# Kernel optimization log

Hardware: AMD Instinct MI355X
Metric: run time of the kernel (lower is better)

## Reference

```python
import jax, jax.numpy as jnp
import numpy as np

B, CH, N = 4, 128, 4096
PC = CH // 2  # pos channels = 64


def setup_inputs() -> dict:
    key = jax.random.key(0)
    ks = jax.random.split(key, 6)
    s_p = 1.0 / np.sqrt(PC)
    s_v = 1.0 / np.sqrt(CH)
    return {
        "pos_bot": jax.random.normal(ks[0], (B, PC, N), dtype=jnp.float32),
        "corr_feats": jax.random.normal(ks[1], (B, CH, N), dtype=jnp.float32),
        "Wp": jax.random.uniform(ks[2], (PC, PC), jnp.float32, -s_p, s_p),
        "bp": jax.random.uniform(ks[3], (PC,), jnp.float32, -s_p, s_p),
        "Wv": jax.random.uniform(ks[4], (CH, CH), jnp.float32, -s_v, s_v),
        "bv": jax.random.uniform(ks[5], (CH,), jnp.float32, -s_v, s_v),
        "beta": jnp.asarray([1.0], dtype=jnp.float32),
    }


def reference(pos_bot, corr_feats, Wp, bp, Wv, bv, beta):
    # 1x1 Conv1d == per-position matmul over channels
    pos = jnp.einsum("oc,bcn->bon", Wp, pos_bot) + bp[None, :, None]      # [B,64,N]
    value = jnp.einsum("oc,bcn->bon", Wv, corr_feats) + bv[None, :, None]  # [B,128,N]

    x = jnp.transpose(pos, (0, 2, 1))  # [B,N,64]
    # squared euclidean pairwise distance: ||xi||^2 + ||xj||^2 - 2 xi.xj
    sq = jnp.sum(x * x, axis=-1)  # [B,N]
    d2 = sq[:, :, None] + sq[:, None, :] - 2.0 * jnp.einsum("bnd,bmd->bnm", x, x)
    d2 = jnp.maximum(d2, 0.0)
    kernel = jnp.exp(-d2 * beta[0])  # [B,N,N] Gaussian RBF

    equation_F = jnp.transpose(value, (0, 2, 1))  # [B,N,128]
    return kernel, equation_F
```

## Files before the change

### kernel.cpp

```cpp
#include <hip/hip_runtime.h>
#include <hip/hip_bf16.h>

typedef _Float16 f16x8 __attribute__((ext_vector_type(8)));
typedef _Float16 f16x4 __attribute__((ext_vector_type(4)));
typedef float    f32x4 __attribute__((ext_vector_type(4)));

constexpr int BB = 4;
constexpr int CH = 128;
constexpr int PC = 64;
constexpr int NN = 4096;

__global__ __launch_bounds__(256) void proj_kernel(
    const float* __restrict__ pos_bot,
    const float* __restrict__ corr,
    const float* __restrict__ Wp,
    const float* __restrict__ bp,
    const float* __restrict__ Wv,
    const float* __restrict__ bv,
    _Float16* __restrict__ xbuf,
    float*    __restrict__ sq,
    float*    __restrict__ eqF)
{
    const int tid  = threadIdx.x;
    const int wid  = tid >> 6;
    const int lane = tid & 63;
    const int l15  = lane & 15;
    const int lg   = lane >> 4;
    const int b    = blockIdx.y & 3;
    const int n    = blockIdx.x * 16 + l15;

    if ((blockIdx.y >> 2) == 0) {
        const int mt = wid;
        f16x8 wf[2], pb[2];
#pragma unroll
        for (int ks = 0; ks < 2; ++ks) {
            const float* wp = Wp + (mt * 16 + l15) * PC + ks * 32 + lg * 8;
            f32x4 w0 = *reinterpret_cast<const f32x4*>(wp);
            f32x4 w1 = *reinterpret_cast<const f32x4*>(wp + 4);
            f16x8 f;
#pragma unroll
            for (int e = 0; e < 4; ++e) { f[e] = (_Float16)w0[e]; f[e + 4] = (_Float16)w1[e]; }
            wf[ks] = f;
            f16x8 g;
#pragma unroll
            for (int e = 0; e < 8; ++e) {
                const int c = ks * 32 + lg * 8 + e;
                g[e] = (_Float16)pos_bot[((size_t)(b * PC + c)) * NN + n];
            }
            pb[ks] = g;
        }

        f32x4 acc = {0.f, 0.f, 0.f, 0.f};
        acc = __builtin_amdgcn_mfma_f32_16x16x32_f16(wf[0], pb[0], acc, 0, 0, 0);
        acc = __builtin_amdgcn_mfma_f32_16x16x32_f16(wf[1], pb[1], acc, 0, 0, 0);

        float partial = 0.f;
        f16x4 h4;
#pragma unroll
        for (int r = 0; r < 4; ++r) {
            const int o = mt * 16 + lg * 4 + r;
            const float v = acc[r] + bp[o];
            const _Float16 h = (_Float16)v;
            h4[r] = h;
            const float hf = (float)h;
            partial = fmaf(hf, hf, partial);
        }
        *reinterpret_cast<f16x4*>(xbuf + ((size_t)(b * NN + n)) * PC + mt * 16 + lg * 4) = h4;

        partial += __shfl_xor(partial, 16);
        partial += __shfl_xor(partial, 32);
        __shared__ float psum[4][16];
        if (lane < 16) psum[wid][l15] = partial;
        __syncthreads();
        if (tid < 16)
            sq[b * NN + blockIdx.x * 16 + tid] =
                psum[0][tid] + psum[1][tid] + psum[2][tid] + psum[3][tid];
        return;
    }

    f16x8 cb[4];
#pragma unroll
    for (int ks = 0; ks < 4; ++ks) {
        f16x8 g;
#pragma unroll
        for (int e = 0; e < 8; ++e) {
            const int c = ks * 32 + lg * 8 + e;
            g[e] = (_Float16)corr[((size_t)(b * CH + c)) * NN + n];
        }
        cb[ks] = g;
    }
#pragma unroll
    for (int half = 0; half < 2; ++half) {
        const int ot = wid + half * 4;
        f32x4 acc = {0.f, 0.f, 0.f, 0.f};
#pragma unroll
        for (int ks = 0; ks < 4; ++ks) {
            const float* wv = Wv + (ot * 16 + l15) * CH + ks * 32 + lg * 8;
            f32x4 w0 = *reinterpret_cast<const f32x4*>(wv);
            f32x4 w1 = *reinterpret_cast<const f32x4*>(wv + 4);
            f16x8 f;
#pragma unroll
            for (int e = 0; e < 4; ++e) { f[e] = (_Float16)w0[e]; f[e + 4] = (_Float16)w1[e]; }
            acc = __builtin_amdgcn_mfma_f32_16x16x32_f16(f, cb[ks], acc, 0, 0, 0);
        }
        f32x4 o4;
#pragma unroll
        for (int r = 0; r < 4; ++r) o4[r] = acc[r] + bv[ot * 16 + lg * 4 + r];
        __builtin_nontemporal_store(
            o4, reinterpret_cast<f32x4*>(eqF + ((size_t)(b * NN + n)) * CH + ot * 16 + lg * 4));
    }
}

__global__ __launch_bounds__(256) void gram_kernel(
    const _Float16* __restrict__ xbuf,
    const float*    __restrict__ sq,
    const float*    __restrict__ beta,
    float*          __restrict__ out)
{
    const int tid  = threadIdx.x;
    const int wid  = tid >> 6;
    const int lane = tid & 63;
    const int l15  = lane & 15;
    const int lg   = lane >> 4;
    const int b    = blockIdx.z;
    const int jb   = blockIdx.x * 512;
    const int rb   = blockIdx.y * 64;
    const int wjb  = jb + wid * 128;

    const _Float16* xb  = xbuf + (size_t)b * NN * PC;
    const float*    sqb = sq + (size_t)b * NN;

    const float bs   = -beta[0] * 1.44269504088896f;
    const float m2bs = -2.f * bs;

    f16x8 bf[8][2];
    float tj[8];
#pragma unroll
    for (int jtf = 0; jtf < 8; ++jtf) {
        const int j = wjb + jtf * 16 + l15;
#pragma unroll
        for (int ks = 0; ks < 2; ++ks)
            bf[jtf][ks] = *reinterpret_cast<const f16x8*>(
                xb + (size_t)j * PC + ks * 32 + lg * 8);
        tj[jtf] = bs * sqb[j];
    }

    __shared__ float lds[4][16][132];

    for (int sl = 0; sl < 4; ++sl) {
        const int ibase = rb + sl * 16;

        const f16x8 af0 = *reinterpret_cast<const f16x8*>(
            xb + (size_t)(ibase + l15) * PC + lg * 8);
        const f16x8 af1 = *reinterpret_cast<const f16x8*>(
            xb + (size_t)(ibase + l15) * PC + 32 + lg * 8);

        f32x4 acc[8];
#pragma unroll
        for (int jtf = 0; jtf < 8; ++jtf) {
            f32x4 z = {0.f, 0.f, 0.f, 0.f};
            acc[jtf] = __builtin_amdgcn_mfma_f32_16x16x32_f16(af0, bf[jtf][0], z, 0, 0, 0);
        }
#pragma unroll
        for (int jtf = 0; jtf < 8; ++jtf)
            acc[jtf] = __builtin_amdgcn_mfma_f32_16x16x32_f16(af1, bf[jtf][1], acc[jtf], 0, 0, 0);

        const f32x4 sv = *reinterpret_cast<const f32x4*>(sqb + ibase + lg * 4);

#pragma unroll
        for (int jtf = 0; jtf < 8; ++jtf) {
#pragma unroll
            for (int r = 0; r < 4; ++r) {
                const float ti = bs * sv[r];
                float arg = fminf(fmaf(m2bs, acc[jtf][r], ti + tj[jtf]), 0.f);
                lds[wid][lg * 4 + r][jtf * 16 + l15] = __builtin_amdgcn_exp2f(arg);
            }
        }

#pragma unroll
        for (int k = 0; k < 8; ++k) {
            const int row = 2 * k + (lane >> 5);
            const int col = (lane & 31) * 4;
            const f32x4 v = *reinterpret_cast<const f32x4*>(&lds[wid][row][col]);
            __builtin_nontemporal_store(
                v, reinterpret_cast<f32x4*>(
                       out + ((size_t)(b * NN + ibase + row)) * NN + wjb + col));
        }
    }
}

extern "C" void kernel_launch(void* const* d_in, const int* in_sizes, int n_in,
                              void* d_out, int out_size, void* d_ws, size_t ws_size,
                              hipStream_t stream) {
    const float* pos_bot = (const float*)d_in[0];
    const float* corr    = (const float*)d_in[1];
    const float* Wp      = (const float*)d_in[2];
    const float* bp      = (const float*)d_in[3];
    const float* Wv      = (const float*)d_in[4];
    const float* bv      = (const float*)d_in[5];
    const float* beta    = (const float*)d_in[6];

    float* out = (float*)d_out;
    float* eqF = out + (size_t)BB * NN * NN;

    _Float16* xbuf = (_Float16*)d_ws;
    float* sq = (float*)((char*)d_ws + (size_t)BB * NN * PC * sizeof(_Float16));

    proj_kernel<<<dim3(NN / 16, 2 * BB), 256, 0, stream>>>(
        pos_bot, corr, Wp, bp, Wv, bv, xbuf, sq, eqF);

    gram_kernel<<<dim3(NN / 512, NN / 64, BB), 256, 0, stream>>>(
        xbuf, sq, beta, out);
}
```

Baseline: 70.38 us.

## Fuse projection into gram kernel, recomputing pos projection per block

Merges the projection and gram kernels into one launch. Value-projection blocks come first, and gram blocks recompute the pos projection for their row and column tiles in registers and LDS, so the xbuf/sq workspace round trip and the second launch go away. The clamp of the distance argument to zero is also dropped. In exchange, pos_bot is read and projected redundantly across many blocks: each gram block reprojects 576 rows from strided fp32 loads. The kernel also now needs more LDS and registers, with launch bounds set to 3 blocks per CU.

```diff
diff --git a/kernel.cpp b/kernel.cpp
--- a/kernel.cpp
+++ b/kernel.cpp
@@ -10,28 +10,78 @@
 constexpr int PC = 64;
 constexpr int NN = 4096;
 
-__global__ __launch_bounds__(256) void proj_kernel(
+__global__ __launch_bounds__(256, 3) void fused_kernel(
     const float* __restrict__ pos_bot,
     const float* __restrict__ corr,
     const float* __restrict__ Wp,
     const float* __restrict__ bp,
     const float* __restrict__ Wv,
     const float* __restrict__ bv,
-    _Float16* __restrict__ xbuf,
-    float*    __restrict__ sq,
-    float*    __restrict__ eqF)
+    const float* __restrict__ beta,
+    float*       __restrict__ out,
+    float*       __restrict__ eqF)
 {
+    const int bid  = blockIdx.x;
     const int tid  = threadIdx.x;
     const int wid  = tid >> 6;
     const int lane = tid & 63;
     const int l15  = lane & 15;
     const int lg   = lane >> 4;
-    const int b    = blockIdx.y & 3;
-    const int n    = blockIdx.x * 16 + l15;
-
-    if ((blockIdx.y >> 2) == 0) {
-        const int mt = wid;
-        f16x8 wf[2], pb[2];
+
+    __shared__ _Float16 ldsA[64][72];
+    __shared__ float    sqA[64];
+    __shared__ float    ldsT[4][16][132];
+
+    if (bid < 1024) {
+        const int b = bid >> 8;
+        const int n = (bid & 255) * 16 + l15;
+
+        f16x8 cb[4];
+#pragma unroll
+        for (int ks = 0; ks < 4; ++ks) {
+            f16x8 g;
+#pragma unroll
+            for (int e = 0; e < 8; ++e) {
+                const int c = ks * 32 + lg * 8 + e;
+                g[e] = (_Float16)corr[((size_t)(b * CH + c)) * NN + n];
+            }
+            cb[ks] = g;
+        }
+#pragma unroll
+        for (int half = 0; half < 2; ++half) {
+            const int ot = wid + half * 4;
+            f32x4 acc = {0.f, 0.f, 0.f, 0.f};
+#pragma unroll
+            for (int ks = 0; ks < 4; ++ks) {
+                const float* wv = Wv + (ot * 16 + l15) * CH + ks * 32 + lg * 8;
+                f32x4 w0 = *reinterpret_cast<const f32x4*>(wv);
+                f32x4 w1 = *reinterpret_cast<const f32x4*>(wv + 4);
+                f16x8 f;
+#pragma unroll
+                for (int e = 0; e < 4; ++e) { f[e] = (_Float16)w0[e]; f[e + 4] = (_Float16)w1[e]; }
+                acc = __builtin_amdgcn_mfma_f32_16x16x32_f16(f, cb[ks], acc, 0, 0, 0);
+            }
+            f32x4 o4;
+#pragma unroll
+            for (int r = 0; r < 4; ++r) o4[r] = acc[r] + bv[ot * 16 + lg * 4 + r];
+            __builtin_nontemporal_store(
+                o4, reinterpret_cast<f32x4*>(eqF + ((size_t)(b * NN + n)) * CH + ot * 16 + lg * 4));
+        }
+        return;
+    }
+
+    const int gid = bid - 1024;
+    const int jb  = (gid & 7) * 512;
+    const int rb  = ((gid >> 3) & 63) * 64;
+    const int b   = gid >> 9;
+
+    const float bs   = -beta[0] * 1.44269504088896f;
+    const float m2bs = -2.f * bs;
+
+    f16x8 wfAll[4][2];
+    f32x4 bpv[4];
+#pragma unroll
+    for (int mt = 0; mt < 4; ++mt) {
 #pragma unroll
         for (int ks = 0; ks < 2; ++ks) {
             const float* wp = Wp + (mt * 16 + l15) * PC + ks * 32 + lg * 8;
@@ -40,120 +90,72 @@
             f16x8 f;
 #pragma unroll
             for (int e = 0; e < 4; ++e) { f[e] = (_Float16)w0[e]; f[e + 4] = (_Float16)w1[e]; }
-            wf[ks] = f;
+            wfAll[mt][ks] = f;
+        }
+        bpv[mt] = *reinterpret_cast<const f32x4*>(bp + mt * 16 + lg * 4);
+    }
+
+    auto project16 = [&](int n0, _Float16* dst, float& tres) {
+        f16x8 pb[2];
+#pragma unroll
+        for (int ks = 0; ks < 2; ++ks) {
             f16x8 g;
 #pragma unroll
             for (int e = 0; e < 8; ++e) {
                 const int c = ks * 32 + lg * 8 + e;
-                g[e] = (_Float16)pos_bot[((size_t)(b * PC + c)) * NN + n];
+                g[e] = (_Float16)pos_bot[((size_t)(b * PC + c)) * NN + (n0 + l15)];
             }
             pb[ks] = g;
         }
-
-        f32x4 acc = {0.f, 0.f, 0.f, 0.f};
-        acc = __builtin_amdgcn_mfma_f32_16x16x32_f16(wf[0], pb[0], acc, 0, 0, 0);
-        acc = __builtin_amdgcn_mfma_f32_16x16x32_f16(wf[1], pb[1], acc, 0, 0, 0);
-
         float partial = 0.f;
-        f16x4 h4;
-#pragma unroll
-        for (int r = 0; r < 4; ++r) {
-            const int o = mt * 16 + lg * 4 + r;
-            const float v = acc[r] + bp[o];
-            const _Float16 h = (_Float16)v;
-            h4[r] = h;
-            const float hf = (float)h;
-            partial = fmaf(hf, hf, partial);
-        }
-        *reinterpret_cast<f16x4*>(xbuf + ((size_t)(b * NN + n)) * PC + mt * 16 + lg * 4) = h4;
-
+#pragma unroll
+        for (int mt = 0; mt < 4; ++mt) {
+            f32x4 acc = {0.f, 0.f, 0.f, 0.f};
+            acc = __builtin_amdgcn_mfma_f32_16x16x32_f16(wfAll[mt][0], pb[0], acc, 0, 0, 0);
+            acc = __builtin_amdgcn_mfma_f32_16x16x32_f16(wfAll[mt][1], pb[1], acc, 0, 0, 0);
+            f16x4 h4;
+#pragma unroll
+            for (int r = 0; r < 4; ++r) {
+                const float v = acc[r] + bpv[mt][r];
+                const _Float16 h = (_Float16)v;
+                h4[r] = h;
+                const float hf = (float)h;
+                partial = fmaf(hf, hf, partial);
+            }
+            *reinterpret_cast<f16x4*>(dst + (size_t)l15 * 72 + mt * 16 + lg * 4) = h4;
+        }
         partial += __shfl_xor(partial, 16);
         partial += __shfl_xor(partial, 32);
-        __shared__ float psum[4][16];
-        if (lane < 16) psum[wid][l15] = partial;
-        __syncthreads();
-        if (tid < 16)
-            sq[b * NN + blockIdx.x * 16 + tid] =
-                psum[0][tid] + psum[1][tid] + psum[2][tid] + psum[3][tid];
-        return;
-    }
-
-    f16x8 cb[4];
-#pragma unroll
-    for (int ks = 0; ks < 4; ++ks) {
-        f16x8 g;
-#pragma unroll
-        for (int e = 0; e < 8; ++e) {
-            const int c = ks * 32 + lg * 8 + e;
-            g[e] = (_Float16)corr[((size_t)(b * CH + c)) * NN + n];
-        }
-        cb[ks] = g;
-    }
-#pragma unroll
-    for (int half = 0; half < 2; ++half) {
-        const int ot = wid + half * 4;
-        f32x4 acc = {0.f, 0.f, 0.f, 0.f};
-#pragma unroll
-        for (int ks = 0; ks < 4; ++ks) {
-            const float* wv = Wv + (ot * 16 + l15) * CH + ks * 32 + lg * 8;
-            f32x4 w0 = *reinterpret_cast<const f32x4*>(wv);
-            f32x4 w1 = *reinterpret_cast<const f32x4*>(wv + 4);
-            f16x8 f;
-#pragma unroll
-            for (int e = 0; e < 4; ++e) { f[e] = (_Float16)w0[e]; f[e + 4] = (_Float16)w1[e]; }
-            acc = __builtin_amdgcn_mfma_f32_16x16x32_f16(f, cb[ks], acc, 0, 0, 0);
-        }
-        f32x4 o4;
-#pragma unroll
-        for (int r = 0; r < 4; ++r) o4[r] = acc[r] + bv[ot * 16 + lg * 4 + r];
-        __builtin_nontemporal_store(
-            o4, reinterpret_cast<f32x4*>(eqF + ((size_t)(b * NN + n)) * CH + ot * 16 + lg * 4));
-    }
-}
-
-__global__ __launch_bounds__(256) void gram_kernel(
-    const _Float16* __restrict__ xbuf,
-    const float*    __restrict__ sq,
-    const float*    __restrict__ beta,
-    float*          __restrict__ out)
-{
-    const int tid  = threadIdx.x;
-    const int wid  = tid >> 6;
-    const int lane = tid & 63;
-    const int l15  = lane & 15;
-    const int lg   = lane >> 4;
-    const int b    = blockIdx.z;
-    const int jb   = blockIdx.x * 512;
-    const int rb   = blockIdx.y * 64;
-    const int wjb  = jb + wid * 128;
-
-    const _Float16* xb  = xbuf + (size_t)b * NN * PC;
-    const float*    sqb = sq + (size_t)b * NN;
-
-    const float bs   = -beta[0] * 1.44269504088896f;
-    const float m2bs = -2.f * bs;
-
+        tres = bs * partial;
+    };
+
+    _Float16* scratch = reinterpret_cast<_Float16*>(&ldsT[wid][0][0]);
     f16x8 bf[8][2];
     float tj[8];
 #pragma unroll
-    for (int jtf = 0; jtf < 8; ++jtf) {
-        const int j = wjb + jtf * 16 + l15;
-#pragma unroll
-        for (int ks = 0; ks < 2; ++ks)
-            bf[jtf][ks] = *reinterpret_cast<const f16x8*>(
-                xb + (size_t)j * PC + ks * 32 + lg * 8);
-        tj[jtf] = bs * sqb[j];
-    }
-
-    __shared__ float lds[4][16][132];
+    for (int g8 = 0; g8 < 8; ++g8) {
+        float t;
+        project16(jb + wid * 128 + g8 * 16, scratch, t);
+        tj[g8] = t;
+        bf[g8][0] = *reinterpret_cast<const f16x8*>(scratch + (size_t)l15 * 72 + lg * 8);
+        bf[g8][1] = *reinterpret_cast<const f16x8*>(scratch + (size_t)l15 * 72 + 32 + lg * 8);
+    }
+
+    {
+        float t;
+        project16(rb + wid * 16, &ldsA[wid * 16][0], t);
+        if (lg == 0) sqA[wid * 16 + l15] = t;
+    }
+    __syncthreads();
+
+    const int wjb = jb + wid * 128;
 
     for (int sl = 0; sl < 4; ++sl) {
         const int ibase = rb + sl * 16;
 
-        const f16x8 af0 = *reinterpret_cast<const f16x8*>(
-            xb + (size_t)(ibase + l15) * PC + lg * 8);
-        const f16x8 af1 = *reinterpret_cast<const f16x8*>(
-            xb + (size_t)(ibase + l15) * PC + 32 + lg * 8);
+        const f16x8 af0 = *reinterpret_cast<const f16x8*>(&ldsA[sl * 16 + l15][lg * 8]);
+        const f16x8 af1 = *reinterpret_cast<const f16x8*>(&ldsA[sl * 16 + l15][32 + lg * 8]);
+        const f32x4 tiv = *reinterpret_cast<const f32x4*>(&sqA[sl * 16 + lg * 4]);
 
         f32x4 acc[8];
 #pragma unroll
@@ -165,15 +167,12 @@
         for (int jtf = 0; jtf < 8; ++jtf)
             acc[jtf] = __builtin_amdgcn_mfma_f32_16x16x32_f16(af1, bf[jtf][1], acc[jtf], 0, 0, 0);
 
-        const f32x4 sv = *reinterpret_cast<const f32x4*>(sqb + ibase + lg * 4);
-
 #pragma unroll
         for (int jtf = 0; jtf < 8; ++jtf) {
 #pragma unroll
             for (int r = 0; r < 4; ++r) {
-                const float ti = bs * sv[r];
-                float arg = fminf(fmaf(m2bs, acc[jtf][r], ti + tj[jtf]), 0.f);
-                lds[wid][lg * 4 + r][jtf * 16 + l15] = __builtin_amdgcn_exp2f(arg);
+                const float arg = fmaf(m2bs, acc[jtf][r], tiv[r] + tj[jtf]);
+                ldsT[wid][lg * 4 + r][jtf * 16 + l15] = __builtin_amdgcn_exp2f(arg);
             }
         }
 
@@ -181,7 +180,7 @@
         for (int k = 0; k < 8; ++k) {
             const int row = 2 * k + (lane >> 5);
             const int col = (lane & 31) * 4;
-            const f32x4 v = *reinterpret_cast<const f32x4*>(&lds[wid][row][col]);
+            const f32x4 v = *reinterpret_cast<const f32x4*>(&ldsT[wid][row][col]);
             __builtin_nontemporal_store(
                 v, reinterpret_cast<f32x4*>(
                        out + ((size_t)(b * NN + ibase + row)) * NN + wjb + col));
@@ -203,12 +202,6 @@
     float* out = (float*)d_out;
     float* eqF = out + (size_t)BB * NN * NN;
 
-    _Float16* xbuf = (_Float16*)d_ws;
-    float* sq = (float*)((char*)d_ws + (size_t)BB * NN * PC * sizeof(_Float16));
-
-    proj_kernel<<<dim3(NN / 16, 2 * BB), 256, 0, stream>>>(
-        pos_bot, corr, Wp, bp, Wv, bv, xbuf, sq, eqF);
-
-    gram_kernel<<<dim3(NN / 512, NN / 64, BB), 256, 0, stream>>>(
-        xbuf, sq, beta, out);
+    fused_kernel<<<dim3(1024 + 2048), 256, 0, stream>>>(
+        pos_bot, corr, Wp, bp, Wv, bv, beta, out, eqF);
 }
```

After: 101.1 us. 43.6% more time.
